# Kernel tuning notes

Measured on AMD Instinct MI355X. Metric: run time of the kernel, lower is better.

Reference implementation:

```python
import jax, jax.numpy as jnp
import numpy as np

VOCAB = 50257
D_MODEL = 256
HIDDEN = 512
NUM_CLASSES = 2
BATCH = 64
SEQ = 512
PAD_IDX = 0


def setup_inputs() -> dict:
    key = jax.random.key(0)
    ks = jax.random.split(key, 8)
    input_ids = jax.random.randint(ks[0], (BATCH, SEQ), 0, VOCAB)
    emb = jax.random.normal(ks[1], (VOCAB, D_MODEL), dtype=jnp.float32) * 0.02
    emb = emb.at[PAD_IDX].set(0.0)  # padding_idx row is zero
    s_x = 1.0 / np.sqrt(D_MODEL)
    s_h = 1.0 / np.sqrt(HIDDEN)
    Wx = jax.random.uniform(ks[2], (D_MODEL, 3 * HIDDEN), minval=-s_x, maxval=s_x)
    Wh = jax.random.uniform(ks[3], (HIDDEN, 3 * HIDDEN), minval=-s_h, maxval=s_h)
    bx = jax.random.uniform(ks[4], (3 * HIDDEN,), minval=-s_h, maxval=s_h)
    bh = jax.random.uniform(ks[5], (3 * HIDDEN,), minval=-s_h, maxval=s_h)
    Wo = jax.random.uniform(ks[6], (HIDDEN, NUM_CLASSES), minval=-s_h, maxval=s_h)
    bo = jax.random.uniform(ks[7], (NUM_CLASSES,), minval=-s_h, maxval=s_h)
    return {"input_ids": input_ids, "emb": emb, "Wx": Wx, "Wh": Wh,
            "bx": bx, "bh": bh, "Wo": Wo, "bo": bo}


def reference(input_ids, emb, Wx, Wh, bx, bh, Wo, bo):
    # Embedding lookup: [B, S, D]
    x = emb[input_ids]
    # Precompute input-side gate projections for all timesteps: [B, S, 3H]
    xg = jnp.einsum('bsd,dg->bsg', x, Wx) + bx
    H = Wh.shape[0]
    h0 = jnp.zeros((input_ids.shape[0], H), dtype=x.dtype)

    def step(h, xg_t):
        hg = h @ Wh + bh                    # [B, 3H]
        xr, xz, xn = jnp.split(xg_t, 3, axis=-1)
        hr, hz, hn = jnp.split(hg, 3, axis=-1)
        r = jax.nn.sigmoid(xr + hr)
        z = jax.nn.sigmoid(xz + hz)
        n = jnp.tanh(xn + r * hn)
        h_new = (1.0 - z) * n + z * h
        return h_new, None

    # scan over time; only the last hidden state feeds the classifier head
    h_last, _ = jax.lax.scan(step, h0, jnp.swapaxes(xg, 0, 1))
    # Dropout is identity in eval mode (p=0.5 at train time)
    logits = h_last @ Wo + bo               # [B, num_classes]
    return logits
```

## Files before the change

### kernel.cpp

```cpp
#include <hip/hip_runtime.h>
#include <hip/hip_bf16.h>

#define BATCH   64
#define SEQ     512
#define DMODEL  256
#define HIDDEN  512
#define G3      1536
#define NBLK    128
#define UPB     4
#define CPB     12
#define CHUNK   128
#define NCHUNK  4
#define HSLOT   (HIDDEN * BATCH)

typedef unsigned long long u64;
typedef unsigned int u32;

__global__ __launch_bounds__(512) void prep_wh(const float* __restrict__ Wh,
                                               float* __restrict__ whp) {
    int t = blockIdx.x * 512 + threadIdx.x;
    int k   = t & 511;
    int cb  = t >> 9;
    int c   = cb % 12;
    int blk = cb / 12;
    int u = c & 3, g = c >> 2;
    whp[t] = Wh[(long)k * G3 + g * HIDDEN + blk * UPB + u];
}

__global__ void init_flags(unsigned* flags) {
    __hip_atomic_store(&flags[threadIdx.x], 0u, __ATOMIC_RELAXED,
                       __HIP_MEMORY_SCOPE_AGENT);
}

__global__ __launch_bounds__(256) void xg_gemm(const int* __restrict__ ids,
                                               const float* __restrict__ emb,
                                               const float* __restrict__ Wx,
                                               const float* __restrict__ bx,
                                               float* __restrict__ xgC,
                                               int chunk) {
    __shared__ float Es[64][68];
    __shared__ float Ws[64][68];
    __shared__ int   sids[64];

    const int tid = threadIdx.x;
    const int nb = blockIdx.x;
    const int lt = blockIdx.y;
    const int s  = chunk * CHUNK + lt;
    const int tn = tid & 15;
    const int tm = tid >> 4;

    if (tid < 64) sids[tid] = ids[tid * SEQ + s];
    __syncthreads();

    float acc[4][4];
#pragma unroll
    for (int i = 0; i < 4; ++i)
#pragma unroll
        for (int j = 0; j < 4; ++j) acc[i][j] = 0.f;

    for (int kb = 0; kb < 256; kb += 64) {
#pragma unroll
        for (int p = 0; p < 4; ++p) {
            int b = p * 16 + tm;
            float4 av = *(const float4*)(emb + (long)sids[b] * DMODEL + kb + tn * 4);
            Es[tn * 4 + 0][b] = av.x;
            Es[tn * 4 + 1][b] = av.y;
            Es[tn * 4 + 2][b] = av.z;
            Es[tn * 4 + 3][b] = av.w;
            int krow = p * 16 + tm;
            float4 wv = *(const float4*)(Wx + (long)(kb + krow) * G3 + nb * 64 + tn * 4);
            *(float4*)&Ws[krow][tn * 4] = wv;
        }
        __syncthreads();
#pragma unroll
        for (int k = 0; k < 64; ++k) {
            float4 w4 = *(const float4*)&Ws[k][tm * 4];
            float4 e4 = *(const float4*)&Es[k][tn * 4];
            float ww[4] = {w4.x, w4.y, w4.z, w4.w};
            float ee[4] = {e4.x, e4.y, e4.z, e4.w};
#pragma unroll
            for (int i = 0; i < 4; ++i)
#pragma unroll
                for (int j = 0; j < 4; ++j)
                    acc[i][j] = fmaf(ww[i], ee[j], acc[i][j]);
        }
        __syncthreads();
    }

#pragma unroll
    for (int i = 0; i < 4; ++i) {
        int col = nb * 64 + tm * 4 + i;
        float bxi = bx[col];
        float4 o;
        o.x = acc[i][0] + bxi;
        o.y = acc[i][1] + bxi;
        o.z = acc[i][2] + bxi;
        o.w = acc[i][3] + bxi;
        *(float4*)(xgC + (long)col * (CHUNK * BATCH) + lt * 64 + tn * 4) = o;
    }
}

__global__ __launch_bounds__(512, 2) void gru_scan(const float* __restrict__ whp,
                                                   const float* __restrict__ xgC,
                                                   const float* __restrict__ bh,
                                                   float* hist,
                                                   unsigned* flags,
                                                   int chunk) {
    const int tid = threadIdx.x;
    const int blk = blockIdx.x;
    const int b   = tid & 63;
    const int wu  = __builtin_amdgcn_readfirstlane(tid >> 6);

    __shared__ float part[2][8][CPB][64];

    const float* wb = whp + blk * (CPB * HIDDEN) + wu * 64;
    const int base = chunk * CHUNK;

    int jg = 0;
    float bhr = 0.f, bhz = 0.f, bhn = 0.f, hprev = 0.f;
    const float* xr_p = nullptr; const float* xz_p = nullptr; const float* xn_p = nullptr;
    if (wu < 4) {
        jg  = blk * UPB + wu;
        bhr = bh[jg];
        bhz = bh[HIDDEN + jg];
        bhn = bh[2 * HIDDEN + jg];
        xr_p = xgC + (long)jg * (CHUNK * BATCH) + b;
        xz_p = xgC + (long)(HIDDEN + jg) * (CHUNK * BATCH) + b;
        xn_p = xgC + (long)(2 * HIDDEN + jg) * (CHUNK * BATCH) + b;
        hprev = (chunk == 0) ? 0.f : hist[(long)jg * 64 + b];
    }

#pragma unroll 1
    for (int lt = 0; lt < CHUNK; ++lt) {
        const int t  = base + lt;
        const int pb = lt & 1;
        const float* hq = hist + (long)lt * HSLOT + wu * (64 * 64) + b;
        float*       hw = hist + (long)((lt + 1) & (CHUNK - 1)) * HSLOT;

        float xr = 0.f, xz = 0.f, xn = 0.f;
        if (wu < 4) {
            xr = xr_p[lt * 64];
            xz = xz_p[lt * 64];
            xn = xn_p[lt * 64];
        }

        float acc[CPB];
#pragma unroll
        for (int c = 0; c < CPB; ++c) acc[c] = 0.f;

        if (t > 0) {
            if (lt > 0) {
                const u32 tgt = (u32)t;
                for (;;) {
                    u32 f = __hip_atomic_load(&flags[wu * 64 + b], __ATOMIC_RELAXED,
                                              __HIP_MEMORY_SCOPE_AGENT);
                    if (__all((int)(f >= tgt))) break;
                    __builtin_amdgcn_s_sleep(1);
                }
            }
            asm volatile("" ::: "memory");
            float hv[64];
#pragma unroll
            for (int i = 0; i < 64; ++i)
                hv[i] = hq[i * 64];
            __builtin_amdgcn_sched_barrier(0);
#pragma unroll
            for (int i = 0; i < 64; ++i) {
                const float hvv = hv[i];
#pragma unroll
                for (int c = 0; c < CPB; ++c)
                    acc[c] = fmaf(hvv, wb[c * HIDDEN + i], acc[c]);
            }
        }

#pragma unroll
        for (int c = 0; c < CPB; ++c) part[pb][wu][c][b] = acc[c];
        __syncthreads();

        if (wu < 4) {
            __builtin_amdgcn_s_setprio(1);
            float hgr = bhr, hgz = bhz, hgn = bhn;
#pragma unroll
            for (int ww = 0; ww < 8; ++ww) {
                hgr += part[pb][ww][wu][b];
                hgz += part[pb][ww][4 + wu][b];
                hgn += part[pb][ww][8 + wu][b];
            }
            float r  = 1.f / (1.f + expf(-(xr + hgr)));
            float z  = 1.f / (1.f + expf(-(xz + hgz)));
            float nn = tanhf(xn + r * hgn);
            float hnew = (1.f - z) * nn + z * hprev;
            hprev = hnew;
            __hip_atomic_store((u32*)hw + (long)jg * 64 + b, __float_as_uint(hnew),
                               __ATOMIC_RELAXED, __HIP_MEMORY_SCOPE_AGENT);
            asm volatile("s_waitcnt vmcnt(0)" ::: "memory");
            if (b == 0)
                __hip_atomic_store(&flags[jg], (u32)(t + 1), __ATOMIC_RELAXED,
                                   __HIP_MEMORY_SCOPE_AGENT);
            __builtin_amdgcn_s_setprio(0);
        }
    }
}

__global__ void head_kernel(const float* __restrict__ hist,
                            const float* __restrict__ Wo,
                            const float* __restrict__ bo,
                            float* __restrict__ out) {
    int tid = threadIdx.x;
    int b = tid >> 1, n = tid & 1;
    float acc = bo[n];
#pragma unroll 8
    for (int k = 0; k < HIDDEN; ++k)
        acc = fmaf(hist[(long)k * 64 + b], Wo[k * 2 + n], acc);
    out[b * 2 + n] = acc;
}

extern "C" void kernel_launch(void* const* d_in, const int* in_sizes, int n_in,
                              void* d_out, int out_size, void* d_ws, size_t ws_size,
                              hipStream_t stream) {
    (void)in_sizes; (void)n_in; (void)out_size; (void)ws_size;
    const int*   ids = (const int*)  d_in[0];
    const float* emb = (const float*)d_in[1];
    const float* Wx  = (const float*)d_in[2];
    const float* Wh  = (const float*)d_in[3];
    const float* bx  = (const float*)d_in[4];
    const float* bh  = (const float*)d_in[5];
    const float* Wo  = (const float*)d_in[6];
    const float* bo  = (const float*)d_in[7];
    float* out = (float*)d_out;

    char* ws = (char*)d_ws;
    unsigned* flags = (unsigned*)ws;
    float* hist = (float*)(ws + 2048);
    float* whp  = (float*)(ws + 2048 + (size_t)CHUNK * HSLOT * 4);
    float* xgC  = (float*)(ws + 2048 + (size_t)CHUNK * HSLOT * 4
                           + (size_t)NBLK * CPB * HIDDEN * 4);

    init_flags<<<dim3(1), dim3(512), 0, stream>>>(flags);
    prep_wh<<<dim3(1536), dim3(512), 0, stream>>>(Wh, whp);
    for (int c = 0; c < NCHUNK; ++c) {
        xg_gemm<<<dim3(24, CHUNK), dim3(256), 0, stream>>>(ids, emb, Wx, bx, xgC, c);
        gru_scan<<<dim3(NBLK), dim3(512), 0, stream>>>(whp, xgC, bh, hist, flags, c);
    }
    head_kernel<<<dim3(1), dim3(128), 0, stream>>>(hist, Wo, bo, out);
}
```

Before: 5.536 ms.

## Partition GRU scan into batch groups with smaller per-group sync and LDS-staged hidden state

Splits the 64-sequence batch into 8 independent groups of 8 sequences, each handled by 16 blocks that together cover the 512 hidden units. Each block now syncs only with the 16 blocks in its own group instead of all 128. Each block stages the group's hidden state in LDS through dedicated loader waves, which also do the flag polling. Every lane computes one full 512-long dot product from L2-resident weights instead of keeping a register-heavy, sliced partial-sum scheme. This is meant to cut global synchronisation fan-in and per-step load latency, at the cost of rereading weights from cache on every step, with 768-thread blocks and a reorganised history layout.

```diff
diff --git a/kernel.cpp b/kernel.cpp
--- a/kernel.cpp
+++ b/kernel.cpp
@@ -6,12 +6,16 @@
 #define DMODEL  256
 #define HIDDEN  512
 #define G3      1536
-#define NBLK    128
-#define UPB     4
-#define CPB     12
 #define CHUNK   128
 #define NCHUNK  4
-#define HSLOT   (HIDDEN * BATCH)
+
+#define GROUPS  8
+#define SPG     8
+#define BPG     16
+#define UPB     32
+#define CPBK    96
+#define HSLOTG  (HIDDEN * SPG)
+#define HGSTRIDE ((long)CHUNK * HSLOTG)
 
 typedef unsigned long long u64;
 typedef unsigned int u32;
@@ -19,12 +23,12 @@
 __global__ __launch_bounds__(512) void prep_wh(const float* __restrict__ Wh,
                                                float* __restrict__ whp) {
     int t = blockIdx.x * 512 + threadIdx.x;
-    int k   = t & 511;
-    int cb  = t >> 9;
-    int c   = cb % 12;
-    int blk = cb / 12;
-    int u = c & 3, g = c >> 2;
-    whp[t] = Wh[(long)k * G3 + g * HIDDEN + blk * UPB + u];
+    int k  = t & 511;
+    int cb = t >> 9;
+    int c  = cb % CPBK;
+    int p  = cb / CPBK;
+    int gate = c >> 5, u = c & 31;
+    whp[t] = Wh[(long)k * G3 + gate * HIDDEN + p * UPB + u];
 }
 
 __global__ void init_flags(unsigned* flags) {
@@ -100,105 +104,122 @@
     }
 }
 
-__global__ __launch_bounds__(512, 2) void gru_scan(const float* __restrict__ whp,
+__global__ __launch_bounds__(768, 1) void gru_scan(const float* __restrict__ whp,
                                                    const float* __restrict__ xgC,
                                                    const float* __restrict__ bh,
                                                    float* hist,
                                                    unsigned* flags,
                                                    int chunk) {
     const int tid = threadIdx.x;
-    const int blk = blockIdx.x;
-    const int b   = tid & 63;
-    const int wu  = __builtin_amdgcn_readfirstlane(tid >> 6);
-
-    __shared__ float part[2][8][CPB][64];
-
-    const float* wb = whp + blk * (CPB * HIDDEN) + wu * 64;
+    const int g   = blockIdx.x & 7;
+    const int p   = blockIdx.x >> 3;
+    const int wv  = __builtin_amdgcn_readfirstlane(tid >> 6);
+    const int ln  = tid & 63;
+
+    __shared__ float hl[SPG][516];
+    __shared__ float gl[CPBK][9];
+
+    float* hist_g = hist + (long)g * HGSTRIDE;
+    unsigned* flg = flags + g * 64;
     const int base = chunk * CHUNK;
 
-    int jg = 0;
+    const int c8 = ln >> 3;
+    const int sf = ln & 7;
+    const int cl = wv * 8 + c8;
+    const float* wp = whp + (long)(p * CPBK + cl) * HIDDEN;
+
+    int u = 0, sp = 0, ju = 0;
     float bhr = 0.f, bhz = 0.f, bhn = 0.f, hprev = 0.f;
+    float xr = 0.f, xz = 0.f, xn = 0.f;
     const float* xr_p = nullptr; const float* xz_p = nullptr; const float* xn_p = nullptr;
-    if (wu < 4) {
-        jg  = blk * UPB + wu;
-        bhr = bh[jg];
-        bhz = bh[HIDDEN + jg];
-        bhn = bh[2 * HIDDEN + jg];
-        xr_p = xgC + (long)jg * (CHUNK * BATCH) + b;
-        xz_p = xgC + (long)(HIDDEN + jg) * (CHUNK * BATCH) + b;
-        xn_p = xgC + (long)(2 * HIDDEN + jg) * (CHUNK * BATCH) + b;
-        hprev = (chunk == 0) ? 0.f : hist[(long)jg * 64 + b];
-    }
+    if (wv < 4) {
+        u  = tid & 31;
+        sp = tid >> 5;
+        ju = p * UPB + u;
+        bhr = bh[ju];
+        bhz = bh[HIDDEN + ju];
+        bhn = bh[2 * HIDDEN + ju];
+        const int b = g * SPG + sp;
+        xr_p = xgC + (long)ju * (CHUNK * BATCH) + b;
+        xz_p = xgC + (long)(HIDDEN + ju) * (CHUNK * BATCH) + b;
+        xn_p = xgC + (long)(2 * HIDDEN + ju) * (CHUNK * BATCH) + b;
+        hprev = (chunk == 0) ? 0.f : hist_g[(long)sp * HIDDEN + ju];
+        xr = xr_p[0]; xz = xz_p[0]; xn = xn_p[0];
+    } else if (chunk > 0) {
+        const int j  = tid - 256;
+        const int ss = j >> 6;
+        const int u8 = (j & 63) << 3;
+        const float* src = hist_g + (long)ss * HIDDEN + u8;
+        *(float4*)&hl[ss][u8]     = *(const float4*)(src);
+        *(float4*)&hl[ss][u8 + 4] = *(const float4*)(src + 4);
+    }
+    __syncthreads();
 
 #pragma unroll 1
     for (int lt = 0; lt < CHUNK; ++lt) {
-        const int t  = base + lt;
-        const int pb = lt & 1;
-        const float* hq = hist + (long)lt * HSLOT + wu * (64 * 64) + b;
-        float*       hw = hist + (long)((lt + 1) & (CHUNK - 1)) * HSLOT;
-
-        float xr = 0.f, xz = 0.f, xn = 0.f;
-        if (wu < 4) {
-            xr = xr_p[lt * 64];
-            xz = xz_p[lt * 64];
-            xn = xn_p[lt * 64];
-        }
-
-        float acc[CPB];
-#pragma unroll
-        for (int c = 0; c < CPB; ++c) acc[c] = 0.f;
-
+        const int t = base + lt;
+
+        float acc = 0.f;
         if (t > 0) {
-            if (lt > 0) {
-                const u32 tgt = (u32)t;
-                for (;;) {
-                    u32 f = __hip_atomic_load(&flags[wu * 64 + b], __ATOMIC_RELAXED,
-                                              __HIP_MEMORY_SCOPE_AGENT);
-                    if (__all((int)(f >= tgt))) break;
-                    __builtin_amdgcn_s_sleep(1);
-                }
+#pragma unroll 4
+            for (int k = 0; k < HIDDEN; k += 8) {
+                float4 w0 = *(const float4*)(wp + k);
+                float4 w1 = *(const float4*)(wp + k + 4);
+                float4 h0 = *(const float4*)&hl[sf][k];
+                float4 h1 = *(const float4*)&hl[sf][k + 4];
+                acc = fmaf(h0.x, w0.x, acc);
+                acc = fmaf(h0.y, w0.y, acc);
+                acc = fmaf(h0.z, w0.z, acc);
+                acc = fmaf(h0.w, w0.w, acc);
+                acc = fmaf(h1.x, w1.x, acc);
+                acc = fmaf(h1.y, w1.y, acc);
+                acc = fmaf(h1.z, w1.z, acc);
+                acc = fmaf(h1.w, w1.w, acc);
             }
-            asm volatile("" ::: "memory");
-            float hv[64];
-#pragma unroll
-            for (int i = 0; i < 64; ++i)
-                hv[i] = hq[i * 64];
-            __builtin_amdgcn_sched_barrier(0);
-#pragma unroll
-            for (int i = 0; i < 64; ++i) {
-                const float hvv = hv[i];
-#pragma unroll
-                for (int c = 0; c < CPB; ++c)
-                    acc[c] = fmaf(hvv, wb[c * HIDDEN + i], acc[c]);
-            }
-        }
-
-#pragma unroll
-        for (int c = 0; c < CPB; ++c) part[pb][wu][c][b] = acc[c];
-        __syncthreads();
-
-        if (wu < 4) {
-            __builtin_amdgcn_s_setprio(1);
-            float hgr = bhr, hgz = bhz, hgn = bhn;
-#pragma unroll
-            for (int ww = 0; ww < 8; ++ww) {
-                hgr += part[pb][ww][wu][b];
-                hgz += part[pb][ww][4 + wu][b];
-                hgn += part[pb][ww][8 + wu][b];
-            }
+        }
+        gl[cl][sf] = acc;
+        __syncthreads();
+
+        if (wv < 4) {
+            float hgr = gl[u][sp] + bhr;
+            float hgz = gl[32 + u][sp] + bhz;
+            float hgn = gl[64 + u][sp] + bhn;
             float r  = 1.f / (1.f + expf(-(xr + hgr)));
             float z  = 1.f / (1.f + expf(-(xz + hgz)));
             float nn = tanhf(xn + r * hgn);
             float hnew = (1.f - z) * nn + z * hprev;
             hprev = hnew;
-            __hip_atomic_store((u32*)hw + (long)jg * 64 + b, __float_as_uint(hnew),
+            float* hw = hist_g + (long)((lt + 1) & (CHUNK - 1)) * HSLOTG
+                        + (long)sp * HIDDEN + ju;
+            __hip_atomic_store((u32*)hw, __float_as_uint(hnew),
                                __ATOMIC_RELAXED, __HIP_MEMORY_SCOPE_AGENT);
             asm volatile("s_waitcnt vmcnt(0)" ::: "memory");
-            if (b == 0)
-                __hip_atomic_store(&flags[jg], (u32)(t + 1), __ATOMIC_RELAXED,
-                                   __HIP_MEMORY_SCOPE_AGENT);
-            __builtin_amdgcn_s_setprio(0);
-        }
+            if (ln == 0)
+                __hip_atomic_store(&flg[p * 4 + wv], (u32)(t + 1),
+                                   __ATOMIC_RELAXED, __HIP_MEMORY_SCOPE_AGENT);
+            if (lt + 1 < CHUNK) {
+                xr = xr_p[(lt + 1) * 64];
+                xz = xz_p[(lt + 1) * 64];
+                xn = xn_p[(lt + 1) * 64];
+            }
+        } else if (lt + 1 < CHUNK) {
+            const u32 tgt = (u32)(t + 1);
+            for (;;) {
+                u32 f = __hip_atomic_load(&flg[ln], __ATOMIC_RELAXED,
+                                          __HIP_MEMORY_SCOPE_AGENT);
+                if (__all((int)(f >= tgt))) break;
+                __builtin_amdgcn_s_sleep(1);
+            }
+            asm volatile("" ::: "memory");
+            const int j  = tid - 256;
+            const int ss = j >> 6;
+            const int u8 = (j & 63) << 3;
+            const float* src = hist_g + (long)((lt + 1) & (CHUNK - 1)) * HSLOTG
+                               + (long)ss * HIDDEN + u8;
+            *(float4*)&hl[ss][u8]     = *(const float4*)(src);
+            *(float4*)&hl[ss][u8 + 4] = *(const float4*)(src + 4);
+        }
+        __syncthreads();
     }
 }
 
@@ -208,10 +229,11 @@
                             float* __restrict__ out) {
     int tid = threadIdx.x;
     int b = tid >> 1, n = tid & 1;
+    const float* hrow = hist + (long)(b >> 3) * HGSTRIDE + (long)(b & 7) * HIDDEN;
     float acc = bo[n];
 #pragma unroll 8
     for (int k = 0; k < HIDDEN; ++k)
-        acc = fmaf(hist[(long)k * 64 + b], Wo[k * 2 + n], acc);
+        acc = fmaf(hrow[k], Wo[k * 2 + n], acc);
     out[b * 2 + n] = acc;
 }
 
@@ -232,15 +254,15 @@
     char* ws = (char*)d_ws;
     unsigned* flags = (unsigned*)ws;
     float* hist = (float*)(ws + 2048);
-    float* whp  = (float*)(ws + 2048 + (size_t)CHUNK * HSLOT * 4);
-    float* xgC  = (float*)(ws + 2048 + (size_t)CHUNK * HSLOT * 4
-                           + (size_t)NBLK * CPB * HIDDEN * 4);
+    float* whp  = (float*)(ws + 2048 + (size_t)GROUPS * HGSTRIDE * 4);
+    float* xgC  = (float*)(ws + 2048 + (size_t)GROUPS * HGSTRIDE * 4
+                           + (size_t)BPG * CPBK * HIDDEN * 4);
 
     init_flags<<<dim3(1), dim3(512), 0, stream>>>(flags);
     prep_wh<<<dim3(1536), dim3(512), 0, stream>>>(Wh, whp);
     for (int c = 0; c < NCHUNK; ++c) {
         xg_gemm<<<dim3(24, CHUNK), dim3(256), 0, stream>>>(ids, emb, Wx, bx, xgC, c);
-        gru_scan<<<dim3(NBLK), dim3(512), 0, stream>>>(whp, xgC, bh, hist, flags, c);
+        gru_scan<<<dim3(GROUPS * BPG), dim3(768), 0, stream>>>(whp, xgC, bh, hist, flags, c);
     }
     head_kernel<<<dim3(1), dim3(128), 0, stream>>>(hist, Wo, bo, out);
 }
```

Result: slower. 10.94 ms (+97.7%).

## Restructure GRU scan into 256 single-wave blocks with LDS-resident weights

Applied to the files above, without the earlier changes.

The recurrent scan now runs as 256 one-wavefront blocks, each owning two hidden units across all gates. Each block keeps its Wh slice in LDS and walks the batch in eight groups of eight sequences, double-buffering the h fetch for the next group behind the current FMAs. The cross-wave LDS reduction and __syncthreads are replaced with wave shuffles, and hist is relaid out batch-major per group. The cost is that every block must now poll 256 flags per step, and the per-step serial chain grows because each block handles all 64 sequences itself.

```diff
diff --git a/kernel.cpp b/kernel.cpp
--- a/kernel.cpp
+++ b/kernel.cpp
@@ -6,12 +6,14 @@
 #define DMODEL  256
 #define HIDDEN  512
 #define G3      1536
-#define NBLK    128
-#define UPB     4
-#define CPB     12
 #define CHUNK   128
 #define NCHUNK  4
-#define HSLOT   (HIDDEN * BATCH)
+
+#define GROUPS  8
+#define SPG     8
+#define NBLK    256
+#define HSLOTG  (HIDDEN * SPG)
+#define HGSTRIDE ((long)CHUNK * HSLOTG)
 
 typedef unsigned long long u64;
 typedef unsigned int u32;
@@ -19,12 +21,12 @@
 __global__ __launch_bounds__(512) void prep_wh(const float* __restrict__ Wh,
                                                float* __restrict__ whp) {
     int t = blockIdx.x * 512 + threadIdx.x;
-    int k   = t & 511;
-    int cb  = t >> 9;
-    int c   = cb % 12;
-    int blk = cb / 12;
-    int u = c & 3, g = c >> 2;
-    whp[t] = Wh[(long)k * G3 + g * HIDDEN + blk * UPB + u];
+    int k  = t & 511;
+    int cb = t >> 9;
+    int c   = cb % 6;
+    int blk = cb / 6;
+    int gate = c >> 1, uu = c & 1;
+    whp[t] = Wh[(long)k * G3 + gate * HIDDEN + blk * 2 + uu];
 }
 
 __global__ void init_flags(unsigned* flags) {
@@ -100,106 +102,145 @@
     }
 }
 
-__global__ __launch_bounds__(512, 2) void gru_scan(const float* __restrict__ whp,
-                                                   const float* __restrict__ xgC,
-                                                   const float* __restrict__ bh,
-                                                   float* hist,
-                                                   unsigned* flags,
-                                                   int chunk) {
-    const int tid = threadIdx.x;
+__global__ __launch_bounds__(64) void gru_scan(const float* __restrict__ whp,
+                                               const float* __restrict__ xgC,
+                                               const float* __restrict__ bh,
+                                               float* hist,
+                                               unsigned* flags,
+                                               int chunk) {
+    const int ln  = threadIdx.x;
     const int blk = blockIdx.x;
-    const int b   = tid & 63;
-    const int wu  = __builtin_amdgcn_readfirstlane(tid >> 6);
-
-    __shared__ float part[2][8][CPB][64];
-
-    const float* wb = whp + blk * (CPB * HIDDEN) + wu * 64;
+    const int s   = ln & 7;
+    const int ks  = ln >> 3;
+    const int u0  = blk * 2;
+    const int u1  = blk * 2 + 1;
+
+    __shared__ float wl[48 * 68];
+
+#pragma unroll
+    for (int p = 0; p < 48; ++p) {
+        int c = p % 6, kss = p / 6;
+        wl[p * 68 + ln] = whp[((long)blk * 6 + c) * 512 + kss * 64 + ln];
+    }
+    __syncthreads();
+
+    float bh0 = bh[u0], bh1 = bh[u1];
+    float bh2 = bh[HIDDEN + u0], bh3 = bh[HIDDEN + u1];
+    float bh4 = bh[2 * HIDDEN + u0], bh5 = bh[2 * HIDDEN + u1];
+
     const int base = chunk * CHUNK;
 
-    int jg = 0;
-    float bhr = 0.f, bhz = 0.f, bhn = 0.f, hprev = 0.f;
-    const float* xr_p = nullptr; const float* xz_p = nullptr; const float* xn_p = nullptr;
-    if (wu < 4) {
-        jg  = blk * UPB + wu;
-        bhr = bh[jg];
-        bhz = bh[HIDDEN + jg];
-        bhn = bh[2 * HIDDEN + jg];
-        xr_p = xgC + (long)jg * (CHUNK * BATCH) + b;
-        xz_p = xgC + (long)(HIDDEN + jg) * (CHUNK * BATCH) + b;
-        xn_p = xgC + (long)(2 * HIDDEN + jg) * (CHUNK * BATCH) + b;
-        hprev = (chunk == 0) ? 0.f : hist[(long)jg * 64 + b];
-    }
+    float hp0[GROUPS], hp1[GROUPS];
+#pragma unroll
+    for (int g = 0; g < GROUPS; ++g) {
+        if (chunk == 0) { hp0[g] = 0.f; hp1[g] = 0.f; }
+        else {
+            hp0[g] = hist[(long)g * HGSTRIDE + (long)s * HIDDEN + u0];
+            hp1[g] = hist[(long)g * HGSTRIDE + (long)s * HIDDEN + u1];
+        }
+    }
+
+    float4 hA[16], hB[16];
+
+#define FETCH(DST, G) do {                                                      \
+        const float4* _sp = (const float4*)(hist + ((long)(G) * CHUNK + lt) *   \
+                            HSLOTG + (long)s * HIDDEN + ks * 64);               \
+        _Pragma("unroll")                                                       \
+        for (int j = 0; j < 16; ++j) DST[j] = _sp[j];                           \
+    } while (0)
+
+#define VISIT(G, CUR, NXT) do {                                                 \
+        const int bb = (G) * SPG + s;                                           \
+        float xr0 = xgC[(long)(u0)        * 8192 + lt * 64 + bb];               \
+        float xr1 = xgC[(long)(u1)        * 8192 + lt * 64 + bb];               \
+        float xz0 = xgC[(long)(512 + u0)  * 8192 + lt * 64 + bb];               \
+        float xz1 = xgC[(long)(512 + u1)  * 8192 + lt * 64 + bb];               \
+        float xn0 = xgC[(long)(1024 + u0) * 8192 + lt * 64 + bb];               \
+        float xn1 = xgC[(long)(1024 + u1) * 8192 + lt * 64 + bb];               \
+        float a0 = 0.f, a1 = 0.f, a2 = 0.f, a3 = 0.f, a4 = 0.f, a5 = 0.f;      \
+        if (t > 0) {                                                            \
+            _Pragma("unroll")                                                   \
+            for (int j = 0; j < 16; ++j) {                                      \
+                float4 hvj = CUR[j];                                            \
+                float4 w;                                                       \
+                w = *(const float4*)&wl[(ks * 6 + 0) * 68 + 4 * j];             \
+                a0 = fmaf(hvj.x, w.x, a0); a0 = fmaf(hvj.y, w.y, a0);           \
+                a0 = fmaf(hvj.z, w.z, a0); a0 = fmaf(hvj.w, w.w, a0);           \
+                w = *(const float4*)&wl[(ks * 6 + 1) * 68 + 4 * j];             \
+                a1 = fmaf(hvj.x, w.x, a1); a1 = fmaf(hvj.y, w.y, a1);           \
+                a1 = fmaf(hvj.z, w.z, a1); a1 = fmaf(hvj.w, w.w, a1);           \
+                w = *(const float4*)&wl[(ks * 6 + 2) * 68 + 4 * j];             \
+                a2 = fmaf(hvj.x, w.x, a2); a2 = fmaf(hvj.y, w.y, a2);           \
+                a2 = fmaf(hvj.z, w.z, a2); a2 = fmaf(hvj.w, w.w, a2);           \
+                w = *(const float4*)&wl[(ks * 6 + 3) * 68 + 4 * j];             \
+                a3 = fmaf(hvj.x, w.x, a3); a3 = fmaf(hvj.y, w.y, a3);           \
+                a3 = fmaf(hvj.z, w.z, a3); a3 = fmaf(hvj.w, w.w, a3);           \
+                w = *(const float4*)&wl[(ks * 6 + 4) * 68 + 4 * j];             \
+                a4 = fmaf(hvj.x, w.x, a4); a4 = fmaf(hvj.y, w.y, a4);           \
+                a4 = fmaf(hvj.z, w.z, a4); a4 = fmaf(hvj.w, w.w, a4);           \
+                w = *(const float4*)&wl[(ks * 6 + 5) * 68 + 4 * j];             \
+                a5 = fmaf(hvj.x, w.x, a5); a5 = fmaf(hvj.y, w.y, a5);           \
+                a5 = fmaf(hvj.z, w.z, a5); a5 = fmaf(hvj.w, w.w, a5);           \
+            }                                                                   \
+        }                                                                       \
+        if ((G) < 7 && t > 0) { FETCH(NXT, (G) + 1); }                          \
+        a0 += __shfl_xor(a0, 8);  a0 += __shfl_xor(a0, 16); a0 += __shfl_xor(a0, 32); \
+        a1 += __shfl_xor(a1, 8);  a1 += __shfl_xor(a1, 16); a1 += __shfl_xor(a1, 32); \
+        a2 += __shfl_xor(a2, 8);  a2 += __shfl_xor(a2, 16); a2 += __shfl_xor(a2, 32); \
+        a3 += __shfl_xor(a3, 8);  a3 += __shfl_xor(a3, 16); a3 += __shfl_xor(a3, 32); \
+        a4 += __shfl_xor(a4, 8);  a4 += __shfl_xor(a4, 16); a4 += __shfl_xor(a4, 32); \
+        a5 += __shfl_xor(a5, 8);  a5 += __shfl_xor(a5, 16); a5 += __shfl_xor(a5, 32); \
+        float r0 = 1.f / (1.f + expf(-(xr0 + a0 + bh0)));                       \
+        float r1 = 1.f / (1.f + expf(-(xr1 + a1 + bh1)));                       \
+        float z0 = 1.f / (1.f + expf(-(xz0 + a2 + bh2)));                       \
+        float z1 = 1.f / (1.f + expf(-(xz1 + a3 + bh3)));                       \
+        float n0 = tanhf(xn0 + r0 * (a4 + bh4));                                \
+        float n1 = tanhf(xn1 + r1 * (a5 + bh5));                                \
+        float h0n = (1.f - z0) * n0 + z0 * hp0[(G)];                            \
+        float h1n = (1.f - z1) * n1 + z1 * hp1[(G)];                            \
+        hp0[(G)] = h0n; hp1[(G)] = h1n;                                         \
+        if (ks == 0) {                                                          \
+            u64 pk = ((u64)__float_as_uint(h1n) << 32) | (u64)__float_as_uint(h0n); \
+            __hip_atomic_store((u64*)(hist + ((long)(G) * CHUNK + slot_w) *     \
+                               HSLOTG + (long)s * HIDDEN + u0), pk,             \
+                               __ATOMIC_RELAXED, __HIP_MEMORY_SCOPE_AGENT);     \
+        }                                                                       \
+    } while (0)
 
 #pragma unroll 1
     for (int lt = 0; lt < CHUNK; ++lt) {
-        const int t  = base + lt;
-        const int pb = lt & 1;
-        const float* hq = hist + (long)lt * HSLOT + wu * (64 * 64) + b;
-        float*       hw = hist + (long)((lt + 1) & (CHUNK - 1)) * HSLOT;
-
-        float xr = 0.f, xz = 0.f, xn = 0.f;
-        if (wu < 4) {
-            xr = xr_p[lt * 64];
-            xz = xz_p[lt * 64];
-            xn = xn_p[lt * 64];
-        }
-
-        float acc[CPB];
-#pragma unroll
-        for (int c = 0; c < CPB; ++c) acc[c] = 0.f;
+        const int t = base + lt;
+        const int slot_w = (lt + 1) & (CHUNK - 1);
 
         if (t > 0) {
-            if (lt > 0) {
-                const u32 tgt = (u32)t;
-                for (;;) {
-                    u32 f = __hip_atomic_load(&flags[wu * 64 + b], __ATOMIC_RELAXED,
-                                              __HIP_MEMORY_SCOPE_AGENT);
-                    if (__all((int)(f >= tgt))) break;
-                    __builtin_amdgcn_s_sleep(1);
-                }
+            const u32 tgt = (u32)t;
+            for (;;) {
+                u32 f0 = __hip_atomic_load(&flags[ln],       __ATOMIC_RELAXED, __HIP_MEMORY_SCOPE_AGENT);
+                u32 f1 = __hip_atomic_load(&flags[64 + ln],  __ATOMIC_RELAXED, __HIP_MEMORY_SCOPE_AGENT);
+                u32 f2 = __hip_atomic_load(&flags[128 + ln], __ATOMIC_RELAXED, __HIP_MEMORY_SCOPE_AGENT);
+                u32 f3 = __hip_atomic_load(&flags[192 + ln], __ATOMIC_RELAXED, __HIP_MEMORY_SCOPE_AGENT);
+                if (__all((int)(f0 >= tgt && f1 >= tgt && f2 >= tgt && f3 >= tgt))) break;
+                __builtin_amdgcn_s_sleep(1);
             }
             asm volatile("" ::: "memory");
-            float hv[64];
-#pragma unroll
-            for (int i = 0; i < 64; ++i)
-                hv[i] = hq[i * 64];
-            __builtin_amdgcn_sched_barrier(0);
-#pragma unroll
-            for (int i = 0; i < 64; ++i) {
-                const float hvv = hv[i];
-#pragma unroll
-                for (int c = 0; c < CPB; ++c)
-                    acc[c] = fmaf(hvv, wb[c * HIDDEN + i], acc[c]);
-            }
-        }
-
-#pragma unroll
-        for (int c = 0; c < CPB; ++c) part[pb][wu][c][b] = acc[c];
-        __syncthreads();
-
-        if (wu < 4) {
-            __builtin_amdgcn_s_setprio(1);
-            float hgr = bhr, hgz = bhz, hgn = bhn;
-#pragma unroll
-            for (int ww = 0; ww < 8; ++ww) {
-                hgr += part[pb][ww][wu][b];
-                hgz += part[pb][ww][4 + wu][b];
-                hgn += part[pb][ww][8 + wu][b];
-            }
-            float r  = 1.f / (1.f + expf(-(xr + hgr)));
-            float z  = 1.f / (1.f + expf(-(xz + hgz)));
-            float nn = tanhf(xn + r * hgn);
-            float hnew = (1.f - z) * nn + z * hprev;
-            hprev = hnew;
-            __hip_atomic_store((u32*)hw + (long)jg * 64 + b, __float_as_uint(hnew),
-                               __ATOMIC_RELAXED, __HIP_MEMORY_SCOPE_AGENT);
-            asm volatile("s_waitcnt vmcnt(0)" ::: "memory");
-            if (b == 0)
-                __hip_atomic_store(&flags[jg], (u32)(t + 1), __ATOMIC_RELAXED,
-                                   __HIP_MEMORY_SCOPE_AGENT);
-            __builtin_amdgcn_s_setprio(0);
-        }
-    }
+            FETCH(hA, 0);
+        }
+
+        VISIT(0, hA, hB);
+        VISIT(1, hB, hA);
+        VISIT(2, hA, hB);
+        VISIT(3, hB, hA);
+        VISIT(4, hA, hB);
+        VISIT(5, hB, hA);
+        VISIT(6, hA, hB);
+        VISIT(7, hB, hA);
+
+        if (ln == 0)
+            __hip_atomic_store(&flags[blk], (u32)(t + 1),
+                               __ATOMIC_RELEASE, __HIP_MEMORY_SCOPE_AGENT);
+    }
+#undef VISIT
+#undef FETCH
 }
 
 __global__ void head_kernel(const float* __restrict__ hist,
@@ -208,10 +249,11 @@
                             float* __restrict__ out) {
     int tid = threadIdx.x;
     int b = tid >> 1, n = tid & 1;
+    const float* hrow = hist + (long)(b >> 3) * HGSTRIDE + (long)(b & 7) * HIDDEN;
     float acc = bo[n];
 #pragma unroll 8
     for (int k = 0; k < HIDDEN; ++k)
-        acc = fmaf(hist[(long)k * 64 + b], Wo[k * 2 + n], acc);
+        acc = fmaf(hrow[k], Wo[k * 2 + n], acc);
     out[b * 2 + n] = acc;
 }
 
@@ -232,15 +274,15 @@
     char* ws = (char*)d_ws;
     unsigned* flags = (unsigned*)ws;
     float* hist = (float*)(ws + 2048);
-    float* whp  = (float*)(ws + 2048 + (size_t)CHUNK * HSLOT * 4);
-    float* xgC  = (float*)(ws + 2048 + (size_t)CHUNK * HSLOT * 4
-                           + (size_t)NBLK * CPB * HIDDEN * 4);
-
-    init_flags<<<dim3(1), dim3(512), 0, stream>>>(flags);
+    float* whp  = (float*)(ws + 2048 + (size_t)GROUPS * HGSTRIDE * 4);
+    float* xgC  = (float*)(ws + 2048 + (size_t)GROUPS * HGSTRIDE * 4
+                           + (size_t)NBLK * 6 * HIDDEN * 4);
+
+    init_flags<<<dim3(1), dim3(256), 0, stream>>>(flags);
     prep_wh<<<dim3(1536), dim3(512), 0, stream>>>(Wh, whp);
     for (int c = 0; c < NCHUNK; ++c) {
         xg_gemm<<<dim3(24, CHUNK), dim3(256), 0, stream>>>(ids, emb, Wx, bx, xgC, c);
-        gru_scan<<<dim3(NBLK), dim3(512), 0, stream>>>(whp, xgC, bh, hist, flags, c);
+        gru_scan<<<dim3(NBLK), dim3(64), 0, stream>>>(whp, xgC, bh, hist, flags, c);
     }
     head_kernel<<<dim3(1), dim3(128), 0, stream>>>(hist, Wo, bo, out);
 }
```

After: 15.70 ms. 184% more time.
